# Kernel optimization log

Hardware: AMD Instinct MI355X
Metric: run time of the kernel (lower is better)

Reference implementation:

```python
import jax, jax.numpy as jnp
import numpy as np
import math

KMAX = 4
K_FLOOR = 1e-6
NUM_GRAPHS = 32

def _k_lattice():
    r = np.arange(-KMAX, KMAX + 1)
    I, J, Kk = np.meshgrid(r, r, r, indexing='ij')
    lat = np.stack([I, J, Kk], axis=-1).reshape(-1, 3).astype(np.float32)
    lat = lat[np.any(lat != 0, axis=1)]  # exclude k=0 (include_k0=False)
    return jnp.asarray(lat)  # [K,3], K=728

def setup_inputs() -> dict:
    key = jax.random.key(0)
    ks = jax.random.split(key, 10)
    N, B, C, H = 8192, NUM_GRAPHS, 4, 64
    pos = jax.random.uniform(ks[0], (N, 3), dtype=jnp.float32) * 10.0
    batch = jnp.sort(jax.random.randint(ks[1], (N,), 0, B)).astype(jnp.int32)
    cell = jnp.eye(3, dtype=jnp.float32)[None] * 12.0 + 0.2 * jax.random.normal(ks[2], (B, 3, 3), dtype=jnp.float32)
    source = 0.1 * jax.random.normal(ks[3], (N, C), dtype=jnp.float32)
    W1 = jax.random.normal(ks[4], (3, H), dtype=jnp.float32) * (1.0 / math.sqrt(3))
    b1 = jnp.zeros((H,), jnp.float32)
    W2 = jax.random.normal(ks[5], (H, H), dtype=jnp.float32) * (1.0 / math.sqrt(H))
    b2 = jnp.zeros((H,), jnp.float32)
    W3 = jax.random.normal(ks[6], (H, 1), dtype=jnp.float32) * (1.0 / math.sqrt(H))
    b3 = jnp.zeros((1,), jnp.float32)
    return {"pos": pos, "batch": batch, "cell": cell, "source": source,
            "W1": W1, "b1": b1, "W2": W2, "b2": b2, "W3": W3, "b3": b3}

def reference(pos, batch, cell, source, W1, b1, W2, b2, W3, b3):
    two_pi = 2.0 * math.pi
    klat = _k_lattice()                              # [K,3]
    B = cell.shape[0]
    inv_cells = jnp.linalg.inv(cell)                 # [B,3,3]
    # fractional coords and phases
    frac = jnp.einsum('ni,nij->nj', pos, inv_cells[batch])   # [N,3]
    phases = two_pi * (frac @ klat.T)                # [N,K]
    cosP = jnp.cos(phases)
    sinP = jnp.sin(phases)
    # structure factors via segment-sum over graphs
    w_cos = source[:, None, :] * cosP[:, :, None]    # [N,K,C]
    w_sin = source[:, None, :] * sinP[:, :, None]
    S_cos = jax.ops.segment_sum(w_cos, batch, num_segments=B)  # [B,K,C]
    S_sin = jax.ops.segment_sum(w_sin, batch, num_segments=B)
    # k-space radial filter
    k_cart = two_pi * jnp.einsum('kd,bdh->bkh', klat, inv_cells)  # [B,K,3]
    k_norms = jnp.linalg.norm(k_cart, axis=-1)       # [B,K]
    safe_k = jnp.maximum(k_norms, K_FLOOR)
    x0 = jnp.log1p(safe_k)
    feat = jnp.stack([x0, x0 * x0, 1.0 / safe_k], axis=-1)       # [B,K,3]
    h = jax.nn.silu(feat @ W1 + b1)
    h = jax.nn.silu(h @ W2 + b2)
    scale = jax.nn.softplus((h @ W3 + b3)[..., 0])   # [B,K]
    w = (4.0 * math.pi / (safe_k * safe_k)) * scale
    w = jnp.where(k_norms > K_FLOOR, w, 0.0)         # include_k0=False
    volumes = jnp.maximum(jnp.abs(jnp.linalg.det(cell)), K_FLOOR)  # [B]
    # per-atom potential
    t_cos = w[batch] * cosP                          # [N,K]
    t_sin = w[batch] * sinP
    potential = (jnp.einsum('nk,nkc->nc', t_cos, S_cos[batch]) +
                 jnp.einsum('nk,nkc->nc', t_sin, S_sin[batch])) / volumes[batch][:, None]
    atom_energy = 0.5 * jnp.sum(source * potential, axis=-1, keepdims=True)  # [N,1]
    return atom_energy
```

## Files before the change

kernel.cpp:

```cpp
#include <hip/hip_runtime.h>
#include <math.h>

#define N_ATOMS 8192
#define NGRAPH  32
#define KHALF   364
#define TWO_PI  6.28318530717958647692f


__device__ __forceinline__ float silu_f(float x) {
    return x / (1.0f + __expf(-x));
}

__device__ __forceinline__ void screv(float rev, float* s, float* c) {
    float f = rev - floorf(rev);
    *s = __builtin_amdgcn_sinf(f);
    *c = __builtin_amdgcn_cosf(f);
}

__device__ __forceinline__ void inv3x3(const float* __restrict__ c, float* iv, float* detOut) {
    float a00 = c[0], a01 = c[1], a02 = c[2];
    float a10 = c[3], a11 = c[4], a12 = c[5];
    float a20 = c[6], a21 = c[7], a22 = c[8];
    float c00 = a11 * a22 - a12 * a21;
    float c01 = a12 * a20 - a10 * a22;
    float c02 = a10 * a21 - a11 * a20;
    float det = a00 * c00 + a01 * c01 + a02 * c02;
    float r = 1.0f / det;
    iv[0] = c00 * r; iv[1] = (a02 * a21 - a01 * a22) * r; iv[2] = (a01 * a12 - a02 * a11) * r;
    iv[3] = c01 * r; iv[4] = (a00 * a22 - a02 * a20) * r; iv[5] = (a02 * a10 - a00 * a12) * r;
    iv[6] = c02 * r; iv[7] = (a01 * a20 - a00 * a21) * r; iv[8] = (a00 * a11 - a01 * a10) * r;
    *detOut = det;
}

__device__ __forceinline__ int lower_bound_wave(const int* __restrict__ batch, int v, int lane) {
    int x = batch[lane * 128];
    int c1 = __popcll(__ballot(x < v));
    int lo2 = (c1 > 0 ? c1 - 1 : 0) * 128;
    int y = batch[lo2 + lane * 2];
    int c2 = __popcll(__ballot(y < v));
    if (c2 == 0) return lo2;
    int cand = lo2 + 2 * c2;
    return (batch[cand - 1] < v) ? cand : cand - 1;
}

__device__ __forceinline__ void tab_fill(float2* __restrict__ t9, float c1, float s1) {
    float c2 = c1 * c1 - s1 * s1, s2 = 2.f * c1 * s1;
    float c3 = c2 * c1 - s2 * s1, s3 = c2 * s1 + s2 * c1;
    float c4 = c2 * c2 - s2 * s2, s4 = 2.f * c2 * s2;
    t9[4] = make_float2(1.f, 0.f);
    t9[5] = make_float2(c1, s1);
    t9[3] = make_float2(c1, -s1);
    t9[6] = make_float2(c2, s2);
    t9[2] = make_float2(c2, -s2);
    t9[7] = make_float2(c3, s3);
    t9[1] = make_float2(c3, -s3);
    t9[8] = make_float2(c4, s4);
    t9[0] = make_float2(c4, -s4);
}

__global__ __launch_bounds__(256) void kAll(
    const float* __restrict__ cell, const float* __restrict__ pos,
    const int* __restrict__ batch, const float* __restrict__ source,
    const float* __restrict__ W1, const float* __restrict__ b1,
    const float* __restrict__ W2, const float* __restrict__ b2,
    const float* __restrict__ W3, const float* __restrict__ b3,
    float* __restrict__ out)
{
    __shared__ float2 tab[128][3][9];
    __shared__ float4 srcs[128];
    __shared__ float4 partC[3][64];
    __shared__ float4 partS[3][64];
    __shared__ float  comb[256];
    __shared__ int    sbounds[2];
    __shared__ float  lw[64];
    __shared__ float4 lSc[64];
    __shared__ float4 lSs[64];

    int bid = blockIdx.x;
    int tid = threadIdx.x;
    int gb = bid >> 3;
    int b  = bid & 7;

    int pA, jA0, jA1, jB0, jB1, nsegA, nel;
    if (b < 4) { pA = b;     jA0 = 0; jA1 = 5; jB0 = 0; jB1 = 0; nsegA = 45; nel = 45; }
    else       { pA = b - 4; jA0 = 5; jA1 = 9;
                 jB0 = b - 4; jB1 = (b == 7) ? 5 : (b - 3);
                 nsegA = 36; nel = 36 + (jB1 - jB0) * 9; }

    int kl = tid & 63;
    int h  = tid >> 6;

    if (h >= 2) {
        int lb = lower_bound_wave(batch, gb + (h - 2), kl);
        if (kl == 0) sbounds[h - 2] = lb;
    }

    float iv[9]; float det;
    inv3x3(cell + gb * 9, iv, &det);
    float vol = fmaxf(fabsf(det), 1e-6f);

    int el = kl;
    int pe, jje, lle;
    if (el < nsegA) { pe = pA; jje = jA0 + el / 9; lle = el % 9; }
    else            { int e2 = el - nsegA; pe = 4; jje = jB0 + e2 / 9; lle = e2 % 9; }
    int hk = pe * 81 + jje * 9 + lle;
    bool evalid = (el < nel) && (hk < KHALF);

    {
        float fi = (float)(pe - 4);
        float fj = (float)(jje - 4);
        float fl = (float)(lle - 4);
        float kx = TWO_PI * (fi * iv[0] + fj * iv[3] + fl * iv[6]);
        float ky = TWO_PI * (fi * iv[1] + fj * iv[4] + fl * iv[7]);
        float kz = TWO_PI * (fi * iv[2] + fj * iv[5] + fl * iv[8]);
        float kn = sqrtf(kx * kx + ky * ky + kz * kz);
        float sk = fmaxf(kn, 1e-6f);
        float x0 = log1pf(sk);
        float f0 = x0, f1 = x0 * x0, f2 = 1.0f / sk;

        float acc[16];
        #pragma unroll
        for (int j = 0; j < 16; ++j) acc[j] = b2[h * 16 + j];
        for (int i = 0; i < 64; ++i) {
            float a = b1[i] + f0 * W1[i] + f1 * W1[64 + i] + f2 * W1[128 + i];
            float hh = silu_f(a);
            const float* w2row = W2 + i * 64 + h * 16;
            #pragma unroll
            for (int j = 0; j < 16; ++j) acc[j] = fmaf(hh, w2row[j], acc[j]);
        }
        float partial = 0.f;
        #pragma unroll
        for (int j = 0; j < 16; ++j) partial += silu_f(acc[j]) * W3[h * 16 + j];
        comb[tid] = partial;
        __syncthreads();
        if (h == 0) {
            float mlp = b3[0] + comb[kl] + comb[64 + kl] + comb[128 + kl] + comb[192 + kl];
            float sc = (mlp > 20.0f) ? mlp : log1pf(__expf(mlp));
            float wgt = (12.566370614359172954f / (sk * sk)) * sc;
            if (!(kn > 1e-6f)) wgt = 0.0f;
            lw[kl] = evalid ? (wgt / vol) : 0.0f;
        }
    }

    int s0 = sbounds[0], e0 = sbounds[1];

    float4 accC = make_float4(0.f, 0.f, 0.f, 0.f);
    float4 accS = make_float4(0.f, 0.f, 0.f, 0.f);

    for (int base = s0; base < e0; base += 128) {
        int cnt = min(128, e0 - base);
        __syncthreads();
        {
            int a    = tid & 127;
            int dsel = tid >> 7;
            if (a < cnt) {
                int n = base + a;
                float px = pos[n * 3], py = pos[n * 3 + 1], pz = pos[n * 3 + 2];
                int d = dsel;
                float ph = px * iv[d] + py * iv[3 + d] + pz * iv[6 + d];
                float s1, c1; screv(ph, &s1, &c1);
                tab_fill(&tab[a][d][0], c1, s1);
                if (dsel == 0) {
                    float ph2 = px * iv[2] + py * iv[5] + pz * iv[8];
                    float s2_, c2_; screv(ph2, &s2_, &c2_);
                    tab_fill(&tab[a][2][0], c2_, s2_);
                } else {
                    srcs[a] = ((const float4*)source)[n];
                }
            }
        }
        __syncthreads();

        if (evalid) {
            for (int a = h; a < cnt; a += 4) {
                float2 ti = tab[a][0][pe];
                float2 tj = tab[a][1][jje];
                float2 tl = tab[a][2][lle];
                float c12 = ti.x * tj.x - ti.y * tj.y;
                float s12 = ti.x * tj.y + ti.y * tj.x;
                float cv = c12 * tl.x - s12 * tl.y;
                float sv = c12 * tl.y + s12 * tl.x;
                float4 s = srcs[a];
                accC.x = fmaf(s.x, cv, accC.x); accC.y = fmaf(s.y, cv, accC.y);
                accC.z = fmaf(s.z, cv, accC.z); accC.w = fmaf(s.w, cv, accC.w);
                accS.x = fmaf(s.x, sv, accS.x); accS.y = fmaf(s.y, sv, accS.y);
                accS.z = fmaf(s.z, sv, accS.z); accS.w = fmaf(s.w, sv, accS.w);
            }
        }
    }

    if (h > 0) {
        partC[h - 1][kl] = accC;
        partS[h - 1][kl] = accS;
    }
    __syncthreads();
    if (h == 0) {
        #pragma unroll
        for (int qq = 0; qq < 3; ++qq) {
            float4 pc = partC[qq][kl], ps = partS[qq][kl];
            accC.x += pc.x; accC.y += pc.y; accC.z += pc.z; accC.w += pc.w;
            accS.x += ps.x; accS.y += ps.y; accS.z += ps.z; accS.w += ps.w;
        }
        lSc[kl] = accC;
        lSs[kl] = accS;
    }
    __syncthreads();

    int g = 4 - pA;

    for (int n = s0 + tid; n < e0; n += 256) {
        float px = pos[n * 3], py = pos[n * 3 + 1], pz = pos[n * 3 + 2];
        float p1 = px * iv[0] + py * iv[3] + pz * iv[6];
        float p2 = px * iv[1] + py * iv[4] + pz * iv[7];
        float p3 = px * iv[2] + py * iv[5] + pz * iv[8];
        float s1, c1; screv(p1, &s1, &c1);
        float s2, c2; screv(p2, &s2, &c2);
        float s3, c3; screv(p3, &s3, &c3);
        float c3_2 = c3 * c3 - s3 * s3, s3_2 = 2.f * c3 * s3;
        float c3_4 = c3_2 * c3_2 - s3_2 * s3_2, s3_4 = 2.f * c3_2 * s3_2;
        float c2_2 = c2 * c2 - s2 * s2, s2_2 = 2.f * c2 * s2;
        float c2_4 = c2_2 * c2_2 - s2_2 * s2_2, s2_4 = 2.f * c2_2 * s2_2;
        float4 s = ((const float4*)source)[n];

        float acc = 0.f;

        {
            float cg_, sg_;
            if (g == 1)      { cg_ = c1; sg_ = s1; }
            else {
                float c2p = c1 * c1 - s1 * s1, s2p = 2.f * c1 * s1;
                if (g == 2)      { cg_ = c2p; sg_ = s2p; }
                else if (g == 3) { cg_ = c2p * c1 - s2p * s1; sg_ = s2p * c1 + c2p * s1; }
                else             { cg_ = c2p * c2p - s2p * s2p; sg_ = 2.f * c2p * s2p; }
            }
            float ci0 = cg_, si0 = -sg_;

            float ejc, ejs;
            if (jA0 == 0) {
                ejc = ci0 * c2_4 + si0 * s2_4;
                ejs = si0 * c2_4 - ci0 * s2_4;
            } else {
                ejc = ci0 * c2 - si0 * s2;
                ejs = si0 * c2 + ci0 * s2;
            }

            for (int jj = jA0; jj < jA1; ++jj) {
                float fc = ejc * c3_4 + ejs * s3_4;
                float fs = ejs * c3_4 - ejc * s3_4;
                #pragma unroll
                for (int ll = 0; ll < 9; ++ll) {
                    int e = (jj - jA0) * 9 + ll;
                    float4 C  = lSc[e];
                    float4 S4 = lSs[e];
                    float w_ = lw[e];
                    float dc = s.x * C.x  + s.y * C.y  + s.z * C.z  + s.w * C.w;
                    float ds = s.x * S4.x + s.y * S4.y + s.z * S4.z + s.w * S4.w;
                    acc = fmaf(w_, fmaf(fc, dc, fs * ds), acc);
                    float nfc = fc * c3 - fs * s3;
                    fs = fc * s3 + fs * c3;
                    fc = nfc;
                }
                float nejc = ejc * c2 - ejs * s2;
                ejs = ejc * s2 + ejs * c2;
                ejc = nejc;
            }
        }

        if (jB1 > jB0) {
            float ejc = c2_4, ejs = -s2_4;
            for (int t = 0; t < jB0; ++t) {
                float nf = ejc * c2 - ejs * s2;
                ejs = ejc * s2 + ejs * c2;
                ejc = nf;
            }
            for (int jj = jB0; jj < jB1; ++jj) {
                float fc = ejc * c3_4 + ejs * s3_4;
                float fs = ejs * c3_4 - ejc * s3_4;
                #pragma unroll
                for (int ll = 0; ll < 9; ++ll) {
                    int e = nsegA + (jj - jB0) * 9 + ll;
                    float4 C  = lSc[e];
                    float4 S4 = lSs[e];
                    float w_ = lw[e];
                    float dc = s.x * C.x  + s.y * C.y  + s.z * C.z  + s.w * C.w;
                    float ds = s.x * S4.x + s.y * S4.y + s.z * S4.z + s.w * S4.w;
                    acc = fmaf(w_, fmaf(fc, dc, fs * ds), acc);
                    float nfc = fc * c3 - fs * s3;
                    fs = fc * s3 + fs * c3;
                    fc = nfc;
                }
                float nejc = ejc * c2 - ejs * s2;
                ejs = ejc * s2 + ejs * c2;
                ejc = nejc;
            }
        }

        atomicAdd(&out[n], acc);
    }
}

extern "C" void kernel_launch(void* const* d_in, const int* in_sizes, int n_in,
                              void* d_out, int out_size, void* d_ws, size_t ws_size,
                              hipStream_t stream)
{
    const float* pos    = (const float*)d_in[0];
    const int*   batch  = (const int*)d_in[1];
    const float* cell   = (const float*)d_in[2];
    const float* source = (const float*)d_in[3];
    const float* W1 = (const float*)d_in[4];
    const float* b1 = (const float*)d_in[5];
    const float* W2 = (const float*)d_in[6];
    const float* b2 = (const float*)d_in[7];
    const float* W3 = (const float*)d_in[8];
    const float* b3 = (const float*)d_in[9];
    float* out = (float*)d_out;
    (void)d_ws; (void)ws_size;

    kAll<<<dim3(NGRAPH * 8), 256, 0, stream>>>(cell, pos, batch, source,
        W1, b1, W2, b2, W3, b3, out);
}
```

Baseline: 99.15 us.

## Double block size to 512 threads and split work across more waves

Raises the block from 256 to 512 threads. The MLP is split across 8 waves of 8 hidden units each, the phase-table fill gives each of 3 thread groups one dimension, the structure-factor accumulation strides over atoms by 8, and the per-atom potential loop splits k-rows between two half-blocks. The aim is more latency hiding and parallelism, since only 256 blocks run on a large GPU. The cost is more partial-sum reduction, redundant per-atom trig work in the second half-block, and extra atomics on the output.

```diff
diff --git a/kernel.cpp b/kernel.cpp
--- a/kernel.cpp
+++ b/kernel.cpp
@@ -58,7 +58,7 @@
     t9[0] = make_float2(c4, -s4);
 }
 
-__global__ __launch_bounds__(256) void kAll(
+__global__ __launch_bounds__(512) void kAll(
     const float* __restrict__ cell, const float* __restrict__ pos,
     const int* __restrict__ batch, const float* __restrict__ source,
     const float* __restrict__ W1, const float* __restrict__ b1,
@@ -68,9 +68,9 @@
 {
     __shared__ float2 tab[128][3][9];
     __shared__ float4 srcs[128];
-    __shared__ float4 partC[3][64];
-    __shared__ float4 partS[3][64];
-    __shared__ float  comb[256];
+    __shared__ float4 partC[7][64];
+    __shared__ float4 partS[7][64];
+    __shared__ float  comb[512];
     __shared__ int    sbounds[2];
     __shared__ float  lw[64];
     __shared__ float4 lSc[64];
@@ -86,13 +86,15 @@
     else       { pA = b - 4; jA0 = 5; jA1 = 9;
                  jB0 = b - 4; jB1 = (b == 7) ? 5 : (b - 3);
                  nsegA = 36; nel = 36 + (jB1 - jB0) * 9; }
+    int nrows  = (jA1 - jA0) + (jB1 - jB0);
+    int rsplit = (nrows + 1) >> 1;
 
     int kl = tid & 63;
     int h  = tid >> 6;
 
-    if (h >= 2) {
-        int lb = lower_bound_wave(batch, gb + (h - 2), kl);
-        if (kl == 0) sbounds[h - 2] = lb;
+    if (h >= 6) {
+        int lb = lower_bound_wave(batch, gb + (h - 6), kl);
+        if (kl == 0) sbounds[h - 6] = lb;
     }
 
     float iv[9]; float det;
@@ -118,23 +120,25 @@
         float x0 = log1pf(sk);
         float f0 = x0, f1 = x0 * x0, f2 = 1.0f / sk;
 
-        float acc[16];
+        float acc[8];
         #pragma unroll
-        for (int j = 0; j < 16; ++j) acc[j] = b2[h * 16 + j];
+        for (int j = 0; j < 8; ++j) acc[j] = b2[h * 8 + j];
         for (int i = 0; i < 64; ++i) {
             float a = b1[i] + f0 * W1[i] + f1 * W1[64 + i] + f2 * W1[128 + i];
             float hh = silu_f(a);
-            const float* w2row = W2 + i * 64 + h * 16;
+            const float* w2row = W2 + i * 64 + h * 8;
             #pragma unroll
-            for (int j = 0; j < 16; ++j) acc[j] = fmaf(hh, w2row[j], acc[j]);
+            for (int j = 0; j < 8; ++j) acc[j] = fmaf(hh, w2row[j], acc[j]);
         }
         float partial = 0.f;
         #pragma unroll
-        for (int j = 0; j < 16; ++j) partial += silu_f(acc[j]) * W3[h * 16 + j];
+        for (int j = 0; j < 8; ++j) partial += silu_f(acc[j]) * W3[h * 8 + j];
         comb[tid] = partial;
         __syncthreads();
         if (h == 0) {
-            float mlp = b3[0] + comb[kl] + comb[64 + kl] + comb[128 + kl] + comb[192 + kl];
+            float mlp = b3[0];
+            #pragma unroll
+            for (int w = 0; w < 8; ++w) mlp += comb[kl + 64 * w];
             float sc = (mlp > 20.0f) ? mlp : log1pf(__expf(mlp));
             float wgt = (12.566370614359172954f / (sk * sk)) * sc;
             if (!(kn > 1e-6f)) wgt = 0.0f;
@@ -155,15 +159,11 @@
             int dsel = tid >> 7;
             if (a < cnt) {
                 int n = base + a;
-                float px = pos[n * 3], py = pos[n * 3 + 1], pz = pos[n * 3 + 2];
-                int d = dsel;
-                float ph = px * iv[d] + py * iv[3 + d] + pz * iv[6 + d];
-                float s1, c1; screv(ph, &s1, &c1);
-                tab_fill(&tab[a][d][0], c1, s1);
-                if (dsel == 0) {
-                    float ph2 = px * iv[2] + py * iv[5] + pz * iv[8];
-                    float s2_, c2_; screv(ph2, &s2_, &c2_);
-                    tab_fill(&tab[a][2][0], c2_, s2_);
+                if (dsel < 3) {
+                    float px = pos[n * 3], py = pos[n * 3 + 1], pz = pos[n * 3 + 2];
+                    float ph = px * iv[dsel] + py * iv[3 + dsel] + pz * iv[6 + dsel];
+                    float s1, c1; screv(ph, &s1, &c1);
+                    tab_fill(&tab[a][dsel][0], c1, s1);
                 } else {
                     srcs[a] = ((const float4*)source)[n];
                 }
@@ -172,7 +172,7 @@
         __syncthreads();
 
         if (evalid) {
-            for (int a = h; a < cnt; a += 4) {
+            for (int a = h; a < cnt; a += 8) {
                 float2 ti = tab[a][0][pe];
                 float2 tj = tab[a][1][jje];
                 float2 tl = tab[a][2][lle];
@@ -196,7 +196,7 @@
     __syncthreads();
     if (h == 0) {
         #pragma unroll
-        for (int qq = 0; qq < 3; ++qq) {
+        for (int qq = 0; qq < 7; ++qq) {
             float4 pc = partC[qq][kl], ps = partS[qq][kl];
             accC.x += pc.x; accC.y += pc.y; accC.z += pc.z; accC.w += pc.w;
             accS.x += ps.x; accS.y += ps.y; accS.z += ps.z; accS.w += ps.w;
@@ -206,9 +206,13 @@
     }
     __syncthreads();
 
+    int half = tid >> 8;
+    int r0 = half ? rsplit : 0;
+    int r1 = half ? nrows  : rsplit;
     int g = 4 - pA;
 
-    for (int n = s0 + tid; n < e0; n += 256) {
+    for (int na = (tid & 255); s0 + na < e0; na += 256) {
+        int n = s0 + na;
         float px = pos[n * 3], py = pos[n * 3 + 1], pz = pos[n * 3 + 2];
         float p1 = px * iv[0] + py * iv[3] + pz * iv[6];
         float p2 = px * iv[1] + py * iv[4] + pz * iv[7];
@@ -223,6 +227,7 @@
         float4 s = ((const float4*)source)[n];
 
         float acc = 0.f;
+        int rr = 0;
 
         {
             float cg_, sg_;
@@ -244,21 +249,23 @@
                 ejs = si0 * c2 + ci0 * s2;
             }
 
-            for (int jj = jA0; jj < jA1; ++jj) {
-                float fc = ejc * c3_4 + ejs * s3_4;
-                float fs = ejs * c3_4 - ejc * s3_4;
-                #pragma unroll
-                for (int ll = 0; ll < 9; ++ll) {
-                    int e = (jj - jA0) * 9 + ll;
-                    float4 C  = lSc[e];
-                    float4 S4 = lSs[e];
-                    float w_ = lw[e];
-                    float dc = s.x * C.x  + s.y * C.y  + s.z * C.z  + s.w * C.w;
-                    float ds = s.x * S4.x + s.y * S4.y + s.z * S4.z + s.w * S4.w;
-                    acc = fmaf(w_, fmaf(fc, dc, fs * ds), acc);
-                    float nfc = fc * c3 - fs * s3;
-                    fs = fc * s3 + fs * c3;
-                    fc = nfc;
+            for (int jj = jA0; jj < jA1; ++jj, ++rr) {
+                if (rr >= r0 && rr < r1) {
+                    float fc = ejc * c3_4 + ejs * s3_4;
+                    float fs = ejs * c3_4 - ejc * s3_4;
+                    #pragma unroll
+                    for (int ll = 0; ll < 9; ++ll) {
+                        int e = rr * 9 + ll;
+                        float4 C  = lSc[e];
+                        float4 S4 = lSs[e];
+                        float w_ = lw[e];
+                        float dc = s.x * C.x  + s.y * C.y  + s.z * C.z  + s.w * C.w;
+                        float ds = s.x * S4.x + s.y * S4.y + s.z * S4.z + s.w * S4.w;
+                        acc = fmaf(w_, fmaf(fc, dc, fs * ds), acc);
+                        float nfc = fc * c3 - fs * s3;
+                        fs = fc * s3 + fs * c3;
+                        fc = nfc;
+                    }
                 }
                 float nejc = ejc * c2 - ejs * s2;
                 ejs = ejc * s2 + ejs * c2;
@@ -273,21 +280,23 @@
                 ejs = ejc * s2 + ejs * c2;
                 ejc = nf;
             }
-            for (int jj = jB0; jj < jB1; ++jj) {
-                float fc = ejc * c3_4 + ejs * s3_4;
-                float fs = ejs * c3_4 - ejc * s3_4;
-                #pragma unroll
-                for (int ll = 0; ll < 9; ++ll) {
-                    int e = nsegA + (jj - jB0) * 9 + ll;
-                    float4 C  = lSc[e];
-                    float4 S4 = lSs[e];
-                    float w_ = lw[e];
-                    float dc = s.x * C.x  + s.y * C.y  + s.z * C.z  + s.w * C.w;
-                    float ds = s.x * S4.x + s.y * S4.y + s.z * S4.z + s.w * S4.w;
-                    acc = fmaf(w_, fmaf(fc, dc, fs * ds), acc);
-                    float nfc = fc * c3 - fs * s3;
-                    fs = fc * s3 + fs * c3;
-                    fc = nfc;
+            for (int jj = jB0; jj < jB1; ++jj, ++rr) {
+                if (rr >= r0 && rr < r1) {
+                    float fc = ejc * c3_4 + ejs * s3_4;
+                    float fs = ejs * c3_4 - ejc * s3_4;
+                    #pragma unroll
+                    for (int ll = 0; ll < 9; ++ll) {
+                        int e = rr * 9 + ll;
+                        float4 C  = lSc[e];
+                        float4 S4 = lSs[e];
+                        float w_ = lw[e];
+                        float dc = s.x * C.x  + s.y * C.y  + s.z * C.z  + s.w * C.w;
+                        float ds = s.x * S4.x + s.y * S4.y + s.z * S4.z + s.w * S4.w;
+                        acc = fmaf(w_, fmaf(fc, dc, fs * ds), acc);
+                        float nfc = fc * c3 - fs * s3;
+                        fs = fc * s3 + fs * c3;
+                        fc = nfc;
+                    }
                 }
                 float nejc = ejc * c2 - ejs * s2;
                 ejs = ejc * s2 + ejs * c2;
@@ -316,6 +325,6 @@
     float* out = (float*)d_out;
     (void)d_ws; (void)ws_size;
 
-    kAll<<<dim3(NGRAPH * 8), 256, 0, stream>>>(cell, pos, batch, source,
+    kAll<<<dim3(NGRAPH * 8), 512, 0, stream>>>(cell, pos, batch, source,
         W1, b1, W2, b2, W3, b3, out);
 }
```

Measured after the change: 92.97 us. 6.2% less time.
